# Optimization experiments

Hardware: AMD Instinct MI355X
Metric: run time of the kernel (lower is better)

Reference implementation:

```python
import jax, jax.numpy as jnp
import numpy as np
from jax import lax

# Model dims (match init_kwargs config)
HID = 2048      # hidden_size
NH = 64         # num_heads
P = 64          # head_dim
N = 128         # ssm_state_size
G = 1           # n_groups
CS = 256        # chunk_size
K = 4           # conv kernel
D_INNER = NH * P                  # 4096
CONV_DIM = D_INNER + 2 * G * N    # 4352
PROJ = D_INNER + CONV_DIM + NH    # 8512
EPS = 1e-5
BATCH, SEQ = 2, 2048


def setup_inputs() -> dict:
    key = jax.random.key(0)
    ks = jax.random.split(key, 8)
    hidden_states = jax.random.normal(ks[0], (BATCH, SEQ, HID), dtype=jnp.float32)
    W_in = jax.random.normal(ks[1], (PROJ, HID), dtype=jnp.float32) * 0.02
    conv_w = jax.random.normal(ks[2], (CONV_DIM, 1, K), dtype=jnp.float32) * 0.2
    conv_b = jax.random.normal(ks[3], (CONV_DIM,), dtype=jnp.float32) * 0.02
    # dt_bias initialized like inv-softplus of dt in [1e-3, 1e-1]
    dt = jnp.exp(jax.random.uniform(ks[4], (NH,)) * (np.log(0.1) - np.log(0.001)) + np.log(0.001))
    dt_bias = (dt + jnp.log(-jnp.expm1(-dt))).astype(jnp.float32)
    A_log = jnp.log(jnp.arange(1, NH + 1, dtype=jnp.float32))
    D_param = jnp.ones((NH,), dtype=jnp.float32)
    norm_w = jnp.ones((D_INNER,), dtype=jnp.float32)
    W_out = jax.random.normal(ks[5], (HID, D_INNER), dtype=jnp.float32) * 0.02
    return {"hidden_states": hidden_states, "W_in": W_in, "conv_w": conv_w,
            "conv_b": conv_b, "dt_bias": dt_bias, "A_log": A_log,
            "D_param": D_param, "norm_w": norm_w, "W_out": W_out}


def _segsum(x):
    # x: (..., c) -> (..., c, c); seg[i, j] = sum_{j < k <= i} x_k (diag 0), -inf above diag
    T = x.shape[-1]
    xc = jnp.cumsum(x, axis=-1)
    seg = xc[..., :, None] - xc[..., None, :]
    mask = jnp.tril(jnp.ones((T, T), dtype=bool))
    return jnp.where(mask, seg, -jnp.inf)


def _mamba2_forward(hidden_states, W_in, conv_w, conv_b, dt_bias, A_log, D_param, norm_w, W_out):
    B_, L_ = hidden_states.shape[:2]
    proj = hidden_states @ W_in.T                           # (b, l, PROJ)
    z = proj[..., :D_INNER]                                 # gate
    xBC = proj[..., D_INNER:D_INNER + CONV_DIM]
    dt = proj[..., D_INNER + CONV_DIM:]                     # (b, l, NH)

    # depthwise causal conv1d + silu
    xc = lax.conv_general_dilated(
        jnp.transpose(xBC, (0, 2, 1)), conv_w,
        window_strides=(1,), padding=[(K - 1, 0)],
        feature_group_count=CONV_DIM)                        # (b, CONV_DIM, l)
    xc = xc + conv_b[None, :, None]
    xBC = jax.nn.silu(jnp.transpose(xc, (0, 2, 1)))          # (b, l, CONV_DIM)

    x = xBC[..., :D_INNER].reshape(B_, L_, NH, P)
    Bm = xBC[..., D_INNER:D_INNER + G * N].reshape(B_, L_, G, N)
    Cm = xBC[..., D_INNER + G * N:].reshape(B_, L_, G, N)

    dt = jax.nn.softplus(dt + dt_bias)                       # (b, l, NH)
    A = -jnp.exp(A_log)                                      # (NH,)

    Bh = jnp.repeat(Bm, NH // G, axis=2)                     # (b, l, h, n)
    Ch = jnp.repeat(Cm, NH // G, axis=2)

    # ---- chunked SSD scan ----
    nc = L_ // CS
    x_dt = (x * dt[..., None]).reshape(B_, nc, CS, NH, P)    # (b, c, s, h, p)
    B_c = Bh.reshape(B_, nc, CS, NH, N)
    C_c = Ch.reshape(B_, nc, CS, NH, N)
    dA = jnp.transpose((dt * A).reshape(B_, nc, CS, NH), (0, 3, 1, 2))  # (b, h, c, s)
    A_cum = jnp.cumsum(dA, axis=-1)                          # (b, h, c, s)

    Lmat = jnp.exp(_segsum(dA))                              # (b, h, c, s, s)
    Y_diag = jnp.einsum('bclhn,bcshn,bhcls,bcshp->bclhp', C_c, B_c, Lmat, x_dt)

    decay_states = jnp.exp(A_cum[..., -1:] - A_cum)          # (b, h, c, s)
    states = jnp.einsum('bclhn,bhcl,bclhp->bchpn', B_c, decay_states, x_dt)

    da_last = A_cum[..., -1]                                 # (b, h, c)

    def step(prev, inp):
        s_k, d_k = inp                                       # (b,h,p,n), (b,h)
        new = prev * jnp.exp(d_k)[..., None, None] + s_k
        return new, prev

    _, prev_states = lax.scan(step, jnp.zeros((B_, NH, P, N), dtype=x.dtype),
                              (jnp.transpose(states, (1, 0, 2, 3, 4)),
                               jnp.transpose(da_last, (2, 0, 1))))
    prev_states = jnp.transpose(prev_states, (1, 2, 0, 3, 4))  # (b, h, c, p, n)

    Y_off = jnp.einsum('bclhn,bhcpn,bhcl->bclhp', C_c, prev_states, jnp.exp(A_cum))

    y = (Y_diag + Y_off).reshape(B_, L_, NH, P) + D_param[None, None, :, None] * x
    y = y.reshape(B_, L_, D_INNER)

    # gated grouped RMSNorm (norm_before_gate=False): norm(y * silu(z)) * w
    g = y * jax.nn.silu(z)
    gs = D_INNER // G
    gr = g.reshape(B_, L_, G, gs)
    var = jnp.mean(gr * gr, axis=-1, keepdims=True)
    gn = (gr * lax.rsqrt(var + EPS)).reshape(B_, L_, D_INNER) * norm_w

    return gn @ W_out.T                                      # (b, l, HID)


def reference(hidden_states, W_in, conv_w, conv_b, dt_bias, A_log, D_param, norm_w, W_out):
    return _mamba2_forward(hidden_states, W_in, conv_w, conv_b, dt_bias, A_log, D_param, norm_w, W_out)
```

## Files before the change

kernel.cpp:

```cpp
#include <hip/hip_runtime.h>

#define SEQLEN 2048
#define NHEADS 64
#define PDIM 64
#define NSTATE 128
#define CSIZE 256
#define NCHUNK 8
#define DINNER 4096
#define CONVD 4352
#define PROJD 8512

using s8v = __attribute__((ext_vector_type(8))) short;
using f4v = __attribute__((ext_vector_type(4))) float;
using bf8v = __attribute__((ext_vector_type(8))) __bf16;

__device__ __forceinline__ short f2bf(float x) {
  union { float f; unsigned u; } t; t.f = x;
  unsigned r = t.u + 0x7FFFu + ((t.u >> 16) & 1u);
  return (short)(r >> 16);
}
__device__ __forceinline__ float bf2f(short s) {
  union { unsigned u; float f; } t;
  t.u = ((unsigned)(unsigned short)s) << 16;
  return t.f;
}

__device__ __forceinline__ f4v mfma_bf16(s8v a, s8v b, f4v c) {
  return __builtin_amdgcn_mfma_f32_16x16x32_bf16(
      __builtin_bit_cast(bf8v, a), __builtin_bit_cast(bf8v, b), c, 0, 0, 0);
}

__device__ __forceinline__ void gll16(const void* g, void* l) {
  __builtin_amdgcn_global_load_lds(
      (const __attribute__((address_space(1))) unsigned*)g,
      (__attribute__((address_space(3))) unsigned*)l, 16, 0, 0);
}

__global__ __launch_bounds__(256) void cast_bf16_kernel(
    const float* __restrict__ in, short* __restrict__ out, int n4) {
  int i = blockIdx.x * 256 + threadIdx.x;
  if (i < n4) {
    float4 v = ((const float4*)in)[i];
    short4 o;
    o.x = f2bf(v.x); o.y = f2bf(v.y); o.z = f2bf(v.z); o.w = f2bf(v.w);
    ((short4*)out)[i] = o;
  }
}


#define G1_STAGE_A(dst, h, kt) do {                                          \
    _Pragma("unroll")                                                        \
    for (int it_ = 0; it_ < 2; ++it_) {                                      \
      int ci_ = it_ * 512 + tid;                                             \
      int r_ = ci_ >> 3;                                                     \
      int g_ = ((ci_ & 7) ^ (r_ & 7)) << 3;                                  \
      gll16(&A[(size_t)(tm0 + (h) * 128 + r_) * 2048 + (kt) * 64 + g_],      \
            &(dst)[(h) * 8192 + ci_ * 8]);                                   \
    }                                                                        \
  } while (0)

#define G1_STAGE_B(dst, h, kt) do {                                          \
    _Pragma("unroll")                                                        \
    for (int it_ = 0; it_ < 2; ++it_) {                                      \
      int ci_ = it_ * 512 + tid;                                             \
      int r_ = ci_ >> 3;                                                     \
      int g_ = ((ci_ & 7) ^ (r_ & 7)) << 3;                                  \
      int br_ = tn0 + (h) * 128 + r_;                                        \
      if (br_ > 8511) br_ = 8511;       \
      gll16(&B[(size_t)br_ * 2048 + (kt) * 64 + g_],                         \
            &(dst)[(h) * 8192 + ci_ * 8]);                                   \
    }                                                                        \
  } while (0)

#define RD_A(m, ks) \
  (*(const s8v*)&Ad[(wm + (m) * 16 + lr) * 64 + (((ks) * 4 + q) ^ sw7) * 8])
#define RD_B(n, ks) \
  (*(const s8v*)&Bd[(wn + (n) * 16 + lr) * 64 + (((ks) * 4 + q) ^ sw7) * 8])

#define G1_MFMA2(m0, x00, x01, x10, x11) do {                                \
    __builtin_amdgcn_s_setprio(1);                                           \
    _Pragma("unroll") for (int n = 0; n < 4; ++n)                            \
      acc[m0][n] = mfma_bf16(x00, bk0[n], acc[m0][n]);                       \
    _Pragma("unroll") for (int n = 0; n < 4; ++n)                            \
      acc[m0][n] = mfma_bf16(x01, bk1[n], acc[m0][n]);                       \
    _Pragma("unroll") for (int n = 0; n < 4; ++n)                            \
      acc[(m0) + 1][n] = mfma_bf16(x10, bk0[n], acc[(m0) + 1][n]);           \
    _Pragma("unroll") for (int n = 0; n < 4; ++n)                            \
      acc[(m0) + 1][n] = mfma_bf16(x11, bk1[n], acc[(m0) + 1][n]);           \
    __builtin_amdgcn_s_setprio(0);                                           \
  } while (0)

__global__ __launch_bounds__(512, 2) void gemm1_256(
    const short* __restrict__ A, const short* __restrict__ B,
    short* __restrict__ z, short* __restrict__ xbc, float* __restrict__ dtb) {
  const int NT = 32;
  const int bid = blockIdx.x;
  const int sid = (bid & 7) * 68 + (bid >> 3);
  const int panel = sid / 136, rem = sid % 136;
  const int bx = rem >> 2, by = panel * 4 + (rem & 3);
  const int tm0 = by * 256, tn0 = bx * 256;
  __shared__ alignas(16) short lds[65536];
  const int tid = threadIdx.x;
  const int lane = tid & 63, wid = tid >> 6;
  const int wm = (wid >> 2) * 128, wn = (wid & 3) * 64;
  const int lr = lane & 15, q = lane >> 4;
  const int sw7 = lr & 7;

  f4v acc[8][4];
#pragma unroll
  for (int m = 0; m < 8; ++m)
#pragma unroll
    for (int n = 0; n < 4; ++n)
#pragma unroll
      for (int r = 0; r < 4; ++r) acc[m][n][r] = 0.f;

  {
    short* A0 = lds;
    short* B0 = lds + 16384;
    short* B1 = lds + 49152;
    G1_STAGE_A(A0, 0, 0); G1_STAGE_A(A0, 1, 0);
    G1_STAGE_B(B0, 0, 0); G1_STAGE_B(B0, 1, 0);
    G1_STAGE_B(B1, 0, 1); G1_STAGE_B(B1, 1, 1);
    asm volatile("s_waitcnt vmcnt(4)" ::: "memory");
    __builtin_amdgcn_s_barrier();
  }

  for (int t = 0; t < NT; ++t) {
    short* Ad = lds + ((t & 1) << 15);
    short* Bd = Ad + 16384;
    short* An = lds + (((t + 1) & 1) << 15);
    s8v bk0[4], bk1[4];
    {
#pragma unroll
      for (int n = 0; n < 4; ++n) { bk0[n] = RD_B(n, 0); bk1[n] = RD_B(n, 1); }
      s8v a00 = RD_A(0, 0), a01 = RD_A(0, 1);
      s8v a10 = RD_A(1, 0), a11 = RD_A(1, 1);
      if (t + 1 < NT) G1_STAGE_A(An, 0, t + 1);
      __builtin_amdgcn_s_barrier();
      asm volatile("s_waitcnt lgkmcnt(0)" ::: "memory");
      G1_MFMA2(0, a00, a01, a10, a11);
      __builtin_amdgcn_s_barrier();
    }
    {
      s8v a00 = RD_A(2, 0), a01 = RD_A(2, 1);
      s8v a10 = RD_A(3, 0), a11 = RD_A(3, 1);
      if (t + 1 < NT) G1_STAGE_A(An, 1, t + 1);
      __builtin_amdgcn_s_barrier();
      asm volatile("s_waitcnt lgkmcnt(0)" ::: "memory");
      G1_MFMA2(2, a00, a01, a10, a11);
      __builtin_amdgcn_s_barrier();
    }
    {
      s8v a00 = RD_A(4, 0), a01 = RD_A(4, 1);
      s8v a10 = RD_A(5, 0), a11 = RD_A(5, 1);
      if (t + 2 < NT) G1_STAGE_B(Bd, 0, t + 2);
      __builtin_amdgcn_s_barrier();
      asm volatile("s_waitcnt lgkmcnt(0)" ::: "memory");
      G1_MFMA2(4, a00, a01, a10, a11);
      __builtin_amdgcn_s_barrier();
    }
    {
      s8v a00 = RD_A(6, 0), a01 = RD_A(6, 1);
      s8v a10 = RD_A(7, 0), a11 = RD_A(7, 1);
      if (t + 2 < NT) G1_STAGE_B(Bd, 1, t + 2);
      if (t < NT - 2) {
        asm volatile("s_waitcnt vmcnt(4)" ::: "memory");
      } else {
        asm volatile("s_waitcnt vmcnt(0)" ::: "memory");
      }
      __builtin_amdgcn_s_barrier();
      asm volatile("s_waitcnt lgkmcnt(0)" ::: "memory");
      G1_MFMA2(6, a00, a01, a10, a11);
      __builtin_amdgcn_s_barrier();
    }
  }

  if (bx == 33) {
    if (wn == 0) {
#pragma unroll
      for (int m = 0; m < 8; ++m)
#pragma unroll
        for (int n = 0; n < 4; ++n) {
          int col = n * 16 + lr;
#pragma unroll
          for (int r = 0; r < 4; ++r) {
            int row = tm0 + wm + m * 16 + q * 4 + r;
            dtb[(size_t)row * NHEADS + col] = acc[m][n][r];
          }
        }
    }
    return;
  }
  short* outp; int stride, colbase;
  if (bx < 16) { outp = z;   stride = DINNER; colbase = tn0; }
  else         { outp = xbc; stride = CONVD;  colbase = tn0 - DINNER; }
  short* Cs = lds;
  for (int h = 0; h < 2; ++h) {
    __syncthreads();
    if ((wid >> 2) == h) {
#pragma unroll
      for (int m = 0; m < 8; ++m)
#pragma unroll
        for (int n = 0; n < 4; ++n)
#pragma unroll
          for (int r = 0; r < 4; ++r)
            Cs[(m * 16 + q * 4 + r) * 264 + wn + n * 16 + lr] =
                f2bf(acc[m][n][r]);
    }
    __syncthreads();
#pragma unroll
    for (int itr = 0; itr < 8; ++itr) {
      int idx = itr * 512 + tid;
      int r = idx >> 5, c8 = (idx & 31) * 8;
      s8v v = *(const s8v*)&Cs[r * 264 + c8];
      *(s8v*)&outp[(size_t)(tm0 + h * 128 + r) * stride + colbase + c8] = v;
    }
  }
}


#define G2_STAGE_A(dst, h, kt) do {                                          \
    _Pragma("unroll")                                                        \
    for (int it_ = 0; it_ < 2; ++it_) {                                      \
      int ci_ = it_ * 512 + tid;                                             \
      int r_ = ci_ >> 3;                                                     \
      int g_ = ((ci_ & 7) ^ (r_ & 7)) << 3;                                  \
      gll16(&Ag[(size_t)(tm0 + (h) * 128 + r_) * 4096 + (kt) * 64 + g_],     \
            &(dst)[(h) * 8192 + ci_ * 8]);                                   \
    }                                                                        \
  } while (0)

#define G2_STAGE_B(dst, h, kt) do {                                          \
    int ci_ = tid;                                                           \
    int r_ = ci_ >> 3;                                                       \
    int g_ = ((ci_ & 7) ^ (r_ & 7)) << 3;                                    \
    gll16(&Bg[(size_t)(tn0 + (h) * 64 + r_) * 4096 + (kt) * 64 + g_],        \
          &(dst)[(h) * 4096 + ci_ * 8]);                                     \
  } while (0)

#define RD_A2(m, ks) \
  (*(const s8v*)&Ad[(wm + (m) * 16 + lr) * 64 + (((ks) * 4 + q) ^ sw7) * 8])
#define RD_B2(n, ks) \
  (*(const s8v*)&Bd[(wn + (n) * 16 + lr) * 64 + (((ks) * 4 + q) ^ sw7) * 8])

#define G2_MFMA2(m0, x00, x01, x10, x11) do {                                \
    __builtin_amdgcn_s_setprio(1);                                           \
    _Pragma("unroll") for (int n = 0; n < 2; ++n)                            \
      acc[m0][n] = mfma_bf16(x00, bk0[n], acc[m0][n]);                       \
    _Pragma("unroll") for (int n = 0; n < 2; ++n)                            \
      acc[m0][n] = mfma_bf16(x01, bk1[n], acc[m0][n]);                       \
    _Pragma("unroll") for (int n = 0; n < 2; ++n)                            \
      acc[(m0) + 1][n] = mfma_bf16(x10, bk0[n], acc[(m0) + 1][n]);           \
    _Pragma("unroll") for (int n = 0; n < 2; ++n)                            \
      acc[(m0) + 1][n] = mfma_bf16(x11, bk1[n], acc[(m0) + 1][n]);           \
    __builtin_amdgcn_s_setprio(0);                                           \
  } while (0)

__global__ __launch_bounds__(512, 2) void gemm2_256x128(
    const short* __restrict__ Ag, const short* __restrict__ Bg,
    float* __restrict__ C) {
  const int NT = 64;
  const int bid = blockIdx.x;
  const int sid = (bid & 7) * 32 + (bid >> 3);
  const int panel = sid >> 6, rem = sid & 63;
  const int bx = rem >> 2, by = panel * 4 + (rem & 3);
  const int tm0 = by * 256, tn0 = bx * 128;
  __shared__ alignas(16) short lds[49152];
  const int tid = threadIdx.x;
  const int lane = tid & 63, wid = tid >> 6;
  const int wm = (wid >> 2) * 128, wn = (wid & 3) * 32;
  const int lr = lane & 15, q = lane >> 4;
  const int sw7 = lr & 7;

  f4v acc[8][2];
#pragma unroll
  for (int m = 0; m < 8; ++m)
#pragma unroll
    for (int n = 0; n < 2; ++n)
#pragma unroll
      for (int r = 0; r < 4; ++r) acc[m][n][r] = 0.f;

  {
    short* A0 = lds;
    short* B0 = lds + 16384;
    short* B1 = lds + 40960;
    G2_STAGE_A(A0, 0, 0); G2_STAGE_A(A0, 1, 0);
    G2_STAGE_B(B0, 0, 0); G2_STAGE_B(B0, 1, 0);
    G2_STAGE_B(B1, 0, 1); G2_STAGE_B(B1, 1, 1);
    asm volatile("s_waitcnt vmcnt(2)" ::: "memory");
    __builtin_amdgcn_s_barrier();
  }

  for (int t = 0; t < NT; ++t) {
    short* Ad = lds + (t & 1) * 24576;
    short* Bd = Ad + 16384;
    short* An = lds + ((t + 1) & 1) * 24576;
    s8v bk0[2], bk1[2];
    {
#pragma unroll
      for (int n = 0; n < 2; ++n) { bk0[n] = RD_B2(n, 0); bk1[n] = RD_B2(n, 1); }
      s8v a00 = RD_A2(0, 0), a01 = RD_A2(0, 1);
      s8v a10 = RD_A2(1, 0), a11 = RD_A2(1, 1);
      if (t + 1 < NT) G2_STAGE_A(An, 0, t + 1);
      __builtin_amdgcn_s_barrier();
      asm volatile("s_waitcnt lgkmcnt(0)" ::: "memory");
      G2_MFMA2(0, a00, a01, a10, a11);
      __builtin_amdgcn_s_barrier();
    }
    {
      s8v a00 = RD_A2(2, 0), a01 = RD_A2(2, 1);
      s8v a10 = RD_A2(3, 0), a11 = RD_A2(3, 1);
      if (t + 1 < NT) G2_STAGE_A(An, 1, t + 1);
      __builtin_amdgcn_s_barrier();
      asm volatile("s_waitcnt lgkmcnt(0)" ::: "memory");
      G2_MFMA2(2, a00, a01, a10, a11);
      __builtin_amdgcn_s_barrier();
    }
    {
      s8v a00 = RD_A2(4, 0), a01 = RD_A2(4, 1);
      s8v a10 = RD_A2(5, 0), a11 = RD_A2(5, 1);
      if (t + 2 < NT) G2_STAGE_B(Bd, 0, t + 2);
      __builtin_amdgcn_s_barrier();
      asm volatile("s_waitcnt lgkmcnt(0)" ::: "memory");
      G2_MFMA2(4, a00, a01, a10, a11);
      __builtin_amdgcn_s_barrier();
    }
    {
      s8v a00 = RD_A2(6, 0), a01 = RD_A2(6, 1);
      s8v a10 = RD_A2(7, 0), a11 = RD_A2(7, 1);
      if (t + 2 < NT) G2_STAGE_B(Bd, 1, t + 2);
      if (t < NT - 2) {
        asm volatile("s_waitcnt vmcnt(2)" ::: "memory");
      } else {
        asm volatile("s_waitcnt vmcnt(0)" ::: "memory");
      }
      __builtin_amdgcn_s_barrier();
      asm volatile("s_waitcnt lgkmcnt(0)" ::: "memory");
      G2_MFMA2(6, a00, a01, a10, a11);
      __builtin_amdgcn_s_barrier();
    }
  }

#pragma unroll
  for (int m = 0; m < 8; ++m)
#pragma unroll
    for (int n = 0; n < 2; ++n) {
      int r0 = tm0 + wm + m * 16 + q * 4;
      int c0 = tn0 + wn + n * 16 + lr;
#pragma unroll
      for (int r = 0; r < 4; ++r)
        C[(size_t)(r0 + r) * 2048 + c0] = acc[m][n][r];
    }
}

__global__ __launch_bounds__(256) void conv_silu_kernel(
    const short* __restrict__ xbc, const float* __restrict__ conv_w,
    const float* __restrict__ conv_b, short* __restrict__ xBCc) {
  int cc = blockIdx.x * 256 + threadIdx.x;
  int bl = blockIdx.y;
  int b = bl >> 11, l = bl & 2047;
  float4 wv = *(const float4*)&conv_w[cc * 4];
  float wk[4] = {wv.x, wv.y, wv.z, wv.w};
  float acc = conv_b[cc];
  const short* pbase = xbc + (size_t)(b * SEQLEN) * CONVD + cc;
#pragma unroll
  for (int k = 0; k < 4; k++) {
    int ls = l - 3 + k;
    if (ls >= 0) acc += bf2f(pbase[(size_t)ls * CONVD]) * wk[k];
  }
  float sv = acc / (1.f + expf(-acc));
  xBCc[(size_t)bl * CONVD + cc] = f2bf(sv);
}

__global__ __launch_bounds__(256) void dt_kernel(
    float* __restrict__ dtb, const float* __restrict__ dt_bias) {
  int idx = blockIdx.x * 256 + threadIdx.x;
  int hh = idx & 63;
  float v = dtb[idx] + dt_bias[hh];
  dtb[idx] = (v > 20.f) ? v : log1pf(expf(v));
}

__global__ __launch_bounds__(256) void ssd_states_kernel(
    const short* __restrict__ xBCc, const float* __restrict__ dtp,
    const float* __restrict__ A_log, short* __restrict__ states,
    float* __restrict__ da_last) {
  const int blk = blockIdx.x;
  const int h = blk & 63, cc = (blk >> 6) & 7, b = blk >> 9;
  const int tid = threadIdx.x;
  __shared__ float dt_s[CSIZE], Acum[CSIZE], w_s[CSIZE];
  __shared__ float xw[64][64];
  __shared__ float Bt[64][NSTATE];
  const size_t row0 = (size_t)(b * SEQLEN + cc * CSIZE);
  dt_s[tid] = dtp[(row0 + tid) * NHEADS + h];
  __syncthreads();
  if (tid == 0) {
    float Aval = -expf(A_log[h]);
    float s = 0.f;
    for (int i = 0; i < CSIZE; i++) { s += dt_s[i]; Acum[i] = s * Aval; }
    da_last[(size_t)(b * NHEADS + h) * NCHUNK + cc] = Acum[CSIZE - 1];
  }
  __syncthreads();
  float total = Acum[CSIZE - 1];
  w_s[tid] = dt_s[tid] * expf(total - Acum[tid]);
  float acc[4][8];
  for (int a = 0; a < 4; a++) for (int j = 0; j < 8; j++) acc[a][j] = 0.f;
  const int pi = (tid & 15) * 4, ni = (tid >> 4) * 8;
  for (int lt = 0; lt < 4; lt++) {
    __syncthreads();
    for (int i = 0; i < 4; i++) {
      int idx = tid + i * 256;
      int r = idx >> 4, c4 = (idx & 15) << 2;
      short4 v = *(const short4*)&xBCc[(row0 + lt * 64 + r) * CONVD + h * PDIM + c4];
      float wl = w_s[lt * 64 + r];
      xw[r][c4 + 0] = bf2f(v.x) * wl;
      xw[r][c4 + 1] = bf2f(v.y) * wl;
      xw[r][c4 + 2] = bf2f(v.z) * wl;
      xw[r][c4 + 3] = bf2f(v.w) * wl;
    }
    for (int i = 0; i < 8; i++) {
      int idx = tid + i * 256;
      int r = idx >> 5, c4 = (idx & 31) << 2;
      short4 v = *(const short4*)&xBCc[(row0 + lt * 64 + r) * CONVD + DINNER + c4];
      Bt[r][c4 + 0] = bf2f(v.x);
      Bt[r][c4 + 1] = bf2f(v.y);
      Bt[r][c4 + 2] = bf2f(v.z);
      Bt[r][c4 + 3] = bf2f(v.w);
    }
    __syncthreads();
    for (int l = 0; l < 64; l++) {
      float4 xv = *(const float4*)&xw[l][pi];
      float4 b0 = *(const float4*)&Bt[l][ni];
      float4 b1 = *(const float4*)&Bt[l][ni + 4];
      float xa[4] = {xv.x, xv.y, xv.z, xv.w};
      float bb[8] = {b0.x, b0.y, b0.z, b0.w, b1.x, b1.y, b1.z, b1.w};
      for (int a = 0; a < 4; a++)
        for (int j = 0; j < 8; j++)
          acc[a][j] += xa[a] * bb[j];
    }
  }
  const size_t sbase = (((size_t)b * NCHUNK + cc) * NHEADS + h) * (PDIM * NSTATE);
  for (int a = 0; a < 4; a++) {
    short o[8];
    for (int j = 0; j < 8; j++) o[j] = f2bf(acc[a][j]);
    *(s8v*)&states[sbase + (size_t)(pi + a) * NSTATE + ni] = *(const s8v*)o;
  }
}

__global__ __launch_bounds__(256) void scan_kernel(
    short* __restrict__ states, const float* __restrict__ da_last) {
  const int bh = blockIdx.x >> 2, sl = blockIdx.x & 3;
  const int b = bh >> 6, h = bh & 63;
  const int tid = threadIdx.x;
  float prev[8];
  for (int i = 0; i < 8; i++) prev[i] = 0.f;
  for (int c = 0; c < NCHUNK; c++) {
    const size_t base = (((size_t)b * NCHUNK + c) * NHEADS + h) * (PDIM * NSTATE)
                      + sl * 2048;
    const float d = expf(da_last[(size_t)bh * NCHUNK + c]);
    for (int i = 0; i < 8; i++) {
      size_t e = base + tid + i * 256;
      float s = bf2f(states[e]);
      states[e] = f2bf(prev[i]);
      prev[i] = prev[i] * d + s;
    }
  }
}

__global__ __launch_bounds__(256) void ssd_y_kernel(
    const short* __restrict__ xBCc, const float* __restrict__ dtp,
    const float* __restrict__ A_log, const float* __restrict__ D_param,
    const short* __restrict__ prevs, short* __restrict__ y) {
  const int blk = blockIdx.x;
  const int h = blk & 63, cc = (blk >> 6) & 7, b = blk >> 9;
  const int tid = threadIdx.x;
  const int lane = tid & 63, w = tid >> 6;
  const int lr = lane & 15, q = lane >> 4;
  __shared__ float dt_s[CSIZE];
  __shared__ float Acum[CSIZE];
  __shared__ short C_s[64][136];
  __shared__ short BP_s[64][136];
  __shared__ short xdtT[64][72];
  __shared__ short Mt[64][72];
  const size_t row0 = (size_t)(b * SEQLEN + cc * CSIZE);
  dt_s[tid] = dtp[(row0 + tid) * NHEADS + h];
  __syncthreads();
  if (tid == 0) {
    float Aval = -expf(A_log[h]);
    float s = 0.f;
    for (int i = 0; i < CSIZE; i++) { s += dt_s[i]; Acum[i] = s * Aval; }
  }
  const float Dh = D_param[h];
  const size_t prevbase = (((size_t)b * NCHUNK + cc) * NHEADS + h) * (PDIM * NSTATE);
  const int wl0 = w * 16;

  for (int lt = 0; lt < 4; lt++) {
    __syncthreads();
    for (int i = 0; i < 4; i++) {
      int idx = tid + i * 256;
      int r = idx >> 4, c8 = (idx & 15) << 3;
      *(s8v*)&C_s[r][c8] =
          *(const s8v*)&xBCc[(row0 + lt * 64 + r) * CONVD + DINNER + NSTATE + c8];
      *(s8v*)&BP_s[r][c8] = *(const s8v*)&prevs[prevbase + (size_t)r * NSTATE + c8];
    }
    __syncthreads();
    f4v acc[4];
    for (int j = 0; j < 4; j++) for (int r = 0; r < 4; r++) acc[j][r] = 0.f;
    for (int ks = 0; ks < 4; ks++) {
      s8v a = *(const s8v*)&C_s[wl0 + lr][ks * 32 + q * 8];
      for (int j = 0; j < 4; j++) {
        s8v bb = *(const s8v*)&BP_s[j * 16 + lr][ks * 32 + q * 8];
        acc[j] = mfma_bf16(a, bb, acc[j]);
      }
    }
    for (int r = 0; r < 4; r++) {
      float e = __expf(Acum[lt * 64 + wl0 + q * 4 + r]);
      for (int j = 0; j < 4; j++) acc[j][r] *= e;
    }
    for (int st = 0; st <= lt; st++) {
      __syncthreads();
      for (int i = 0; i < 4; i++) {
        int idx = tid + i * 256;
        int r = idx >> 4, c8 = (idx & 15) << 3;
        *(s8v*)&BP_s[r][c8] =
            *(const s8v*)&xBCc[(row0 + st * 64 + r) * CONVD + DINNER + c8];
      }
      for (int i = 0; i < 4; i++) {
        int idx = tid + i * 256;
        int r = idx >> 4, c4 = (idx & 15) << 2;
        float dtv = dt_s[st * 64 + r];
        short4 v = *(const short4*)&xBCc[(row0 + st * 64 + r) * CONVD + h * PDIM + c4];
        xdtT[c4 + 0][r] = f2bf(bf2f(v.x) * dtv);
        xdtT[c4 + 1][r] = f2bf(bf2f(v.y) * dtv);
        xdtT[c4 + 2][r] = f2bf(bf2f(v.z) * dtv);
        xdtT[c4 + 3][r] = f2bf(bf2f(v.w) * dtv);
      }
      __syncthreads();
      f4v sacc[4];
      for (int j = 0; j < 4; j++) for (int r = 0; r < 4; r++) sacc[j][r] = 0.f;
      for (int ks = 0; ks < 4; ks++) {
        s8v a = *(const s8v*)&C_s[wl0 + lr][ks * 32 + q * 8];
        for (int j = 0; j < 4; j++) {
          s8v bb = *(const s8v*)&BP_s[j * 16 + lr][ks * 32 + q * 8];
          sacc[j] = mfma_bf16(a, bb, sacc[j]);
        }
      }
      int lbase = lt * 64 + wl0 + q * 4;
      for (int j = 0; j < 4; j++) {
        int sg = st * 64 + j * 16 + lr;
        for (int r = 0; r < 4; r++) {
          int ll = lbase + r;
          float m = (sg <= ll) ? sacc[j][r] * __expf(Acum[ll] - Acum[sg]) : 0.f;
          Mt[wl0 + q * 4 + r][j * 16 + lr] = f2bf(m);
        }
      }
      __syncthreads();
      for (int ss2 = 0; ss2 < 2; ss2++) {
        s8v a = *(const s8v*)&Mt[wl0 + lr][ss2 * 32 + q * 8];
        for (int j = 0; j < 4; j++) {
          s8v bb = *(const s8v*)&xdtT[j * 16 + lr][ss2 * 32 + q * 8];
          acc[j] = mfma_bf16(a, bb, acc[j]);
        }
      }
    }
    for (int j = 0; j < 4; j++)
      for (int r = 0; r < 4; r++) {
        int lrow = wl0 + q * 4 + r;
        int ll = lt * 64 + lrow;
        int p = j * 16 + lr;
        float xv = bf2f(xBCc[(row0 + ll) * CONVD + h * PDIM + p]);
        Mt[lrow][p] = f2bf(acc[j][r] + Dh * xv);
      }
    __syncthreads();
    for (int ps = 0; ps < 2; ps++) {
      int r = ps * 32 + (tid >> 3);
      int c8 = (tid & 7) * 8;
      s8v v = *(const s8v*)&Mt[r][c8];
      *(s8v*)&y[(row0 + lt * 64 + r) * DINNER + h * PDIM + c8] = v;
    }
  }
}

__global__ __launch_bounds__(256) void norm_cast_kernel(
    const short* __restrict__ y, const short* __restrict__ z,
    const float* __restrict__ norm_w, short* __restrict__ g,
    const float* __restrict__ wsrc, short* __restrict__ wdst) {
  int bl = blockIdx.x, tid = threadIdx.x;
  if (bl >= 4096) {
    int base = (bl - 4096) * 1024 + tid;
#pragma unroll
    for (int i = 0; i < 4; i++) {
      int idx = base + i * 256;
      float4 v = ((const float4*)wsrc)[idx];
      short4 o;
      o.x = f2bf(v.x); o.y = f2bf(v.y); o.z = f2bf(v.z); o.w = f2bf(v.w);
      ((short4*)wdst)[idx] = o;
    }
    return;
  }
  const short4* yrow = (const short4*)(y + (size_t)bl * DINNER);
  const short4* zrow = (const short4*)(z + (size_t)bl * DINNER);
  float gv[16];
  float ss = 0.f;
  for (int i = 0; i < 4; i++) {
    short4 yv = yrow[tid + i * 256];
    short4 zv = zrow[tid + i * 256];
    float zf[4] = {bf2f(zv.x), bf2f(zv.y), bf2f(zv.z), bf2f(zv.w)};
    float yf[4] = {bf2f(yv.x), bf2f(yv.y), bf2f(yv.z), bf2f(yv.w)};
    for (int t = 0; t < 4; t++) {
      float gg = yf[t] * (zf[t] / (1.f + expf(-zf[t])));
      gv[i * 4 + t] = gg;
      ss += gg * gg;
    }
  }
  for (int off = 32; off > 0; off >>= 1) ss += __shfl_down(ss, off);
  __shared__ float red[4];
  __shared__ float rsS;
  if ((tid & 63) == 0) red[tid >> 6] = ss;
  __syncthreads();
  if (tid == 0) rsS = rsqrtf((red[0] + red[1] + red[2] + red[3]) * (1.f / 4096.f) + 1e-5f);
  __syncthreads();
  float rs = rsS;
  for (int i = 0; i < 4; i++) {
    int j4 = (tid + i * 256) * 4;
    float4 nw = *(const float4*)&norm_w[j4];
    short4 o;
    o.x = f2bf(gv[i * 4 + 0] * rs * nw.x);
    o.y = f2bf(gv[i * 4 + 1] * rs * nw.y);
    o.z = f2bf(gv[i * 4 + 2] * rs * nw.z);
    o.w = f2bf(gv[i * 4 + 3] * rs * nw.w);
    *(short4*)&g[(size_t)bl * DINNER + j4] = o;
  }
}

extern "C" void kernel_launch(void* const* d_in, const int* in_sizes, int n_in,
                              void* d_out, int out_size, void* d_ws, size_t ws_size,
                              hipStream_t stream) {
  const float* hidden  = (const float*)d_in[0];
  const float* W_in    = (const float*)d_in[1];
  const float* conv_w  = (const float*)d_in[2];
  const float* conv_b  = (const float*)d_in[3];
  const float* dt_bias = (const float*)d_in[4];
  const float* A_log   = (const float*)d_in[5];
  const float* D_param = (const float*)d_in[6];
  const float* norm_w  = (const float*)d_in[7];
  const float* W_out   = (const float*)d_in[8];
  float* out = (float*)d_out;

  char* ws = (char*)d_ws;
  short* z_bf  = (short*)(ws + 0);
  float* dtb   = (float*)(ws + 33554432);
  float* da_l  = (float*)(ws + 34603008);
  short* xbc_pre = (short*)(ws + 34607104);
  short* y_bf    = (short*)(ws + 34607104);
  short* hid_bf  = (short*)(ws + 70258688);
  short* win_bf  = (short*)(ws + 87035904);
  short* xBCc    = (short*)(ws + 70258688);
  short* states  = (short*)(ws + 105910272);
  short* g_bf    = (short*)(ws + 70258688);
  short* wout_bf = (short*)(ws + 105910272);
  if (ws_size < (size_t)122687488) return;

  cast_bf16_kernel<<<8192, 256, 0, stream>>>(hidden, hid_bf, 2097152);
  cast_bf16_kernel<<<17024, 256, 0, stream>>>(W_in, win_bf, 4358144);

  gemm1_256<<<544, 512, 0, stream>>>(hid_bf, win_bf, z_bf, xbc_pre, dtb);

  conv_silu_kernel<<<dim3(17, 4096), 256, 0, stream>>>(xbc_pre, conv_w, conv_b, xBCc);
  dt_kernel<<<1024, 256, 0, stream>>>(dtb, dt_bias);

  ssd_states_kernel<<<1024, 256, 0, stream>>>(xBCc, dtb, A_log, states, da_l);
  scan_kernel<<<512, 256, 0, stream>>>(states, da_l);
  ssd_y_kernel<<<1024, 256, 0, stream>>>(xBCc, dtb, A_log, D_param, states, y_bf);

  norm_cast_kernel<<<6144, 256, 0, stream>>>(y_bf, z_bf, norm_w, g_bf, W_out, wout_bf);

  gemm2_256x128<<<256, 512, 0, stream>>>(g_bf, wout_bf, out);
}
```

Before: 638.3 us.

## Reorder SSD chunk loops to reuse B/x tiles and register-resident C fragments

The intra-chunk SSD kernel now makes the source sub-tile the outer loop. Each B and x·dt tile is loaded into shared memory once per source tile instead of once per (target, source) pair. The previous-state tile is loaded once per block, and the C fragments plus the accumulators for all four target sub-tiles are held in registers across the whole computation. Separately, the inter-chunk scan kernel switches to 8-wide vectorized loads and stores of state elements. Holding all accumulators and C fragments in registers raises VGPR pressure, which could reduce occupancy.

```diff
diff --git a/kernel.cpp b/kernel.cpp
--- a/kernel.cpp
+++ b/kernel.cpp
@@ -452,17 +452,22 @@
   const int b = bh >> 6, h = bh & 63;
   const int tid = threadIdx.x;
   float prev[8];
+#pragma unroll
   for (int i = 0; i < 8; i++) prev[i] = 0.f;
   for (int c = 0; c < NCHUNK; c++) {
     const size_t base = (((size_t)b * NCHUNK + c) * NHEADS + h) * (PDIM * NSTATE)
                       + sl * 2048;
     const float d = expf(da_last[(size_t)bh * NCHUNK + c]);
+    size_t e0 = base + (size_t)tid * 8;
+    s8v sv = *(const s8v*)&states[e0];
+    short ov[8];
+#pragma unroll
     for (int i = 0; i < 8; i++) {
-      size_t e = base + tid + i * 256;
-      float s = bf2f(states[e]);
-      states[e] = f2bf(prev[i]);
+      float s = bf2f(sv[i]);
+      ov[i] = f2bf(prev[i]);
       prev[i] = prev[i] * d + s;
     }
+    *(s8v*)&states[e0] = *(const s8v*)ov;
   }
 }
 
@@ -477,8 +482,8 @@
   const int lr = lane & 15, q = lane >> 4;
   __shared__ float dt_s[CSIZE];
   __shared__ float Acum[CSIZE];
-  __shared__ short C_s[64][136];
-  __shared__ short BP_s[64][136];
+  __shared__ short PV_s[64][136];
+  __shared__ short B_s[64][136];
   __shared__ short xdtT[64][72];
   __shared__ short Mt[64][72];
   const size_t row0 = (size_t)(b * SEQLEN + cc * CSIZE);
@@ -493,60 +498,77 @@
   const size_t prevbase = (((size_t)b * NCHUNK + cc) * NHEADS + h) * (PDIM * NSTATE);
   const int wl0 = w * 16;
 
+#pragma unroll
+  for (int i = 0; i < 4; i++) {
+    int idx = tid + i * 256;
+    int r = idx >> 4, c8 = (idx & 15) << 3;
+    *(s8v*)&PV_s[r][c8] = *(const s8v*)&prevs[prevbase + (size_t)r * NSTATE + c8];
+  }
+  __syncthreads();
+
+  s8v cfr[4][4];
+  f4v acc[4][4];
+#pragma unroll
   for (int lt = 0; lt < 4; lt++) {
-    __syncthreads();
+#pragma unroll
+    for (int ks = 0; ks < 4; ks++)
+      cfr[lt][ks] = *(const s8v*)&xBCc[(row0 + lt * 64 + wl0 + lr) * CONVD
+                                       + DINNER + NSTATE + ks * 32 + q * 8];
+#pragma unroll
+    for (int j = 0; j < 4; j++)
+#pragma unroll
+      for (int r = 0; r < 4; r++) acc[lt][j][r] = 0.f;
+#pragma unroll
+    for (int ks = 0; ks < 4; ks++)
+#pragma unroll
+      for (int j = 0; j < 4; j++)
+        acc[lt][j] = mfma_bf16(cfr[lt][ks],
+            *(const s8v*)&PV_s[j * 16 + lr][ks * 32 + q * 8], acc[lt][j]);
+#pragma unroll
+    for (int r = 0; r < 4; r++) {
+      float e = __expf(Acum[lt * 64 + wl0 + q * 4 + r]);
+#pragma unroll
+      for (int j = 0; j < 4; j++) acc[lt][j][r] *= e;
+    }
+  }
+
+  for (int st = 0; st < 4; st++) {
+#pragma unroll
     for (int i = 0; i < 4; i++) {
       int idx = tid + i * 256;
       int r = idx >> 4, c8 = (idx & 15) << 3;
-      *(s8v*)&C_s[r][c8] =
-          *(const s8v*)&xBCc[(row0 + lt * 64 + r) * CONVD + DINNER + NSTATE + c8];
-      *(s8v*)&BP_s[r][c8] = *(const s8v*)&prevs[prevbase + (size_t)r * NSTATE + c8];
+      *(s8v*)&B_s[r][c8] =
+          *(const s8v*)&xBCc[(row0 + st * 64 + r) * CONVD + DINNER + c8];
+    }
+#pragma unroll
+    for (int i = 0; i < 4; i++) {
+      int idx = tid + i * 256;
+      int r = idx >> 4, c4 = (idx & 15) << 2;
+      float dtv = dt_s[st * 64 + r];
+      short4 v = *(const short4*)&xBCc[(row0 + st * 64 + r) * CONVD + h * PDIM + c4];
+      xdtT[c4 + 0][r] = f2bf(bf2f(v.x) * dtv);
+      xdtT[c4 + 1][r] = f2bf(bf2f(v.y) * dtv);
+      xdtT[c4 + 2][r] = f2bf(bf2f(v.z) * dtv);
+      xdtT[c4 + 3][r] = f2bf(bf2f(v.w) * dtv);
     }
     __syncthreads();
-    f4v acc[4];
-    for (int j = 0; j < 4; j++) for (int r = 0; r < 4; r++) acc[j][r] = 0.f;
-    for (int ks = 0; ks < 4; ks++) {
-      s8v a = *(const s8v*)&C_s[wl0 + lr][ks * 32 + q * 8];
-      for (int j = 0; j < 4; j++) {
-        s8v bb = *(const s8v*)&BP_s[j * 16 + lr][ks * 32 + q * 8];
-        acc[j] = mfma_bf16(a, bb, acc[j]);
-      }
-    }
-    for (int r = 0; r < 4; r++) {
-      float e = __expf(Acum[lt * 64 + wl0 + q * 4 + r]);
-      for (int j = 0; j < 4; j++) acc[j][r] *= e;
-    }
-    for (int st = 0; st <= lt; st++) {
-      __syncthreads();
-      for (int i = 0; i < 4; i++) {
-        int idx = tid + i * 256;
-        int r = idx >> 4, c8 = (idx & 15) << 3;
-        *(s8v*)&BP_s[r][c8] =
-            *(const s8v*)&xBCc[(row0 + st * 64 + r) * CONVD + DINNER + c8];
-      }
-      for (int i = 0; i < 4; i++) {
-        int idx = tid + i * 256;
-        int r = idx >> 4, c4 = (idx & 15) << 2;
-        float dtv = dt_s[st * 64 + r];
-        short4 v = *(const short4*)&xBCc[(row0 + st * 64 + r) * CONVD + h * PDIM + c4];
-        xdtT[c4 + 0][r] = f2bf(bf2f(v.x) * dtv);
-        xdtT[c4 + 1][r] = f2bf(bf2f(v.y) * dtv);
-        xdtT[c4 + 2][r] = f2bf(bf2f(v.z) * dtv);
-        xdtT[c4 + 3][r] = f2bf(bf2f(v.w) * dtv);
-      }
-      __syncthreads();
+    for (int lt = st; lt < 4; lt++) {
       f4v sacc[4];
-      for (int j = 0; j < 4; j++) for (int r = 0; r < 4; r++) sacc[j][r] = 0.f;
-      for (int ks = 0; ks < 4; ks++) {
-        s8v a = *(const s8v*)&C_s[wl0 + lr][ks * 32 + q * 8];
-        for (int j = 0; j < 4; j++) {
-          s8v bb = *(const s8v*)&BP_s[j * 16 + lr][ks * 32 + q * 8];
-          sacc[j] = mfma_bf16(a, bb, sacc[j]);
-        }
-      }
+#pragma unroll
+      for (int j = 0; j < 4; j++)
+#pragma unroll
+        for (int r = 0; r < 4; r++) sacc[j][r] = 0.f;
+#pragma unroll
+      for (int ks = 0; ks < 4; ks++)
+#pragma unroll
+        for (int j = 0; j < 4; j++)
+          sacc[j] = mfma_bf16(cfr[lt][ks],
+              *(const s8v*)&B_s[j * 16 + lr][ks * 32 + q * 8], sacc[j]);
       int lbase = lt * 64 + wl0 + q * 4;
+#pragma unroll
       for (int j = 0; j < 4; j++) {
         int sg = st * 64 + j * 16 + lr;
+#pragma unroll
         for (int r = 0; r < 4; r++) {
           int ll = lbase + r;
           float m = (sg <= ll) ? sacc[j][r] * __expf(Acum[ll] - Acum[sg]) : 0.f;
@@ -554,29 +576,38 @@
         }
       }
       __syncthreads();
+#pragma unroll
       for (int ss2 = 0; ss2 < 2; ss2++) {
         s8v a = *(const s8v*)&Mt[wl0 + lr][ss2 * 32 + q * 8];
-        for (int j = 0; j < 4; j++) {
-          s8v bb = *(const s8v*)&xdtT[j * 16 + lr][ss2 * 32 + q * 8];
-          acc[j] = mfma_bf16(a, bb, acc[j]);
-        }
+#pragma unroll
+        for (int j = 0; j < 4; j++)
+          acc[lt][j] = mfma_bf16(a,
+              *(const s8v*)&xdtT[j * 16 + lr][ss2 * 32 + q * 8], acc[lt][j]);
       }
     }
+    __syncthreads();
+  }
+
+  for (int lt = 0; lt < 4; lt++) {
+#pragma unroll
     for (int j = 0; j < 4; j++)
+#pragma unroll
       for (int r = 0; r < 4; r++) {
         int lrow = wl0 + q * 4 + r;
         int ll = lt * 64 + lrow;
         int p = j * 16 + lr;
         float xv = bf2f(xBCc[(row0 + ll) * CONVD + h * PDIM + p]);
-        Mt[lrow][p] = f2bf(acc[j][r] + Dh * xv);
+        Mt[lrow][p] = f2bf(acc[lt][j][r] + Dh * xv);
       }
     __syncthreads();
+#pragma unroll
     for (int ps = 0; ps < 2; ps++) {
       int r = ps * 32 + (tid >> 3);
       int c8 = (tid & 7) * 8;
       s8v v = *(const s8v*)&Mt[r][c8];
       *(s8v*)&y[(row0 + lt * 64 + r) * DINNER + h * PDIM + c8] = v;
     }
+    __syncthreads();
   }
 }
 
```

Result: slower. 714.2 us (+11.9%).
